# Kernel optimization log

Measured on AMD Instinct MI355X. Metric: run time of the kernel, lower is better.

The kernel has to match this reference:

```python
import jax, jax.numpy as jnp
import numpy as np
from math import sqrt


def setup_inputs() -> dict:
    key = jax.random.key(0)
    ks = jax.random.split(key, 5)
    B, S, D = 4, 2048, 1024
    scale = 0.02
    return {
        "x": jax.random.normal(ks[0], (B, S, D), dtype=jnp.float32),
        "Wq": jax.random.normal(ks[1], (D, D), dtype=jnp.float32) * scale,
        "Wk": jax.random.normal(ks[2], (D, D), dtype=jnp.float32) * scale,
        "Wv": jax.random.normal(ks[3], (D, D), dtype=jnp.float32) * scale,
        "Wo": jax.random.normal(ks[4], (D, D), dtype=jnp.float32) * scale,
    }


def reference(x, Wq, Wk, Wv, Wo):
    NUM_HEAD = 16
    B, S, D = x.shape
    d_k = D // NUM_HEAD

    # fused QKV projection: weights are (d_model, d_in), applied as W @ x^T -> x @ W^T
    q = jnp.einsum('od,bsd->bso', Wq, x)
    k = jnp.einsum('od,bsd->bso', Wk, x)
    v = jnp.einsum('od,bsd->bso', Wv, x)

    def split_heads(t):  # [B,S,D] -> [B,H,S,d_k]
        return t.reshape(B, S, NUM_HEAD, d_k).transpose(0, 2, 1, 3)

    q, k, v = split_heads(q), split_heads(k), split_heads(v)

    # naive causal attention: full [B,H,S,S] score matrix
    scores = jnp.einsum('bhqd,bhkd->bhqk', q, k) / sqrt(d_k)
    causal = jnp.tril(jnp.ones((S, S), dtype=bool))  # [S,S]
    scores = jnp.where(causal, scores, -jnp.inf)
    probs = jax.nn.softmax(scores, axis=-1)
    attn = jnp.einsum('bhqk,bhkd->bhqd', probs, v)

    # merge heads: [B,H,S,d_k] -> [B,S,D]
    attn = attn.transpose(0, 2, 1, 3).reshape(B, S, D)
    # output projection
    return jnp.einsum('om,bsm->bso', Wo, attn)
```

## Files before the change

### kernel.cpp

```cpp
#include <hip/hip_runtime.h>
#include <hip/hip_bf16.h>
#include <stdint.h>

typedef unsigned short u16;
typedef __attribute__((ext_vector_type(8))) short bf16x8;
typedef __attribute__((ext_vector_type(4))) float f32x4;
typedef __attribute__((ext_vector_type(16))) float f32x16;

#define AS1 __attribute__((address_space(1)))
#define AS3 __attribute__((address_space(3)))

__device__ __forceinline__ u16 f2bf(float f) {
  union { float f; uint32_t u; } v; v.f = f;
  uint32_t u = v.u;
  return (u16)((u + 0x7FFFu + ((u >> 16) & 1u)) >> 16);
}

__device__ __forceinline__ uint32_t cvtpk(float lo, float hi) {
  uint32_t d;
  asm("v_cvt_pk_bf16_f32 %0, %1, %2" : "=v"(d) : "v"(lo), "v"(hi));
  return d;
}

__global__ __launch_bounds__(256) void cvt_all_kernel(const float* __restrict__ x,
    const float* __restrict__ Wq, const float* __restrict__ Wk,
    const float* __restrict__ Wv, const float* __restrict__ Wo,
    u16* __restrict__ xb, u16* __restrict__ wqb, u16* __restrict__ wkb,
    u16* __restrict__ wvb, u16* __restrict__ wob) {
  const int bid = blockIdx.x;
  const float* s;
  u16* d;
  int i;
  if (bid < 8192) {
    s = x; d = xb; i = bid * 256 + threadIdx.x;
  } else {
    const int w = (bid - 8192) >> 10;
    i = ((bid - 8192) & 1023) * 256 + threadIdx.x;
    s = (w == 0) ? Wq : (w == 1) ? Wk : (w == 2) ? Wv : Wo;
    d = (w == 0) ? wqb : (w == 1) ? wkb : (w == 2) ? wvb : wob;
  }
  float4 v = reinterpret_cast<const float4*>(s)[i];
  uint2 o;
  o.x = cvtpk(v.x, v.y);
  o.y = cvtpk(v.z, v.w);
  reinterpret_cast<uint2*>(d)[i] = o;
}

#define QSCALE 0.18033688011112042f

#define GK 64

template <int MODE, int KC, typename OutT>
__device__ __forceinline__ void gemm128_body(u16* __restrict__ lds,
    const u16* __restrict__ A, const u16* __restrict__ Bm, OutT* __restrict__ C,
    int M, int N, int by, int bx, float oscale) {
  const int tid = threadIdx.x;
  const int lane = tid & 63;
  const int wave = tid >> 6;
  const int wm = wave >> 1, wn = wave & 1;
  const int l15 = lane & 15, lhi = lane >> 4;
  const int axor = (lane & 7) << 4;

  const int srow = tid >> 3;
  const int scol = (((tid & 7) ^ (srow & 7)) << 4);
  const size_t Kb = (size_t)KC * 2;
  const uint8_t* Ag = (const uint8_t*)A + (size_t)(by * 128 + srow) * Kb + scol;
  const uint8_t* Bg = (const uint8_t*)Bm + (size_t)(bx * 128 + srow) * Kb + scol;
  uint8_t* Lb = (uint8_t*)lds;

#define STG128(bufi, kt)                                                                  \
  do {                                                                                    \
    _Pragma("unroll") for (int c = 0; c < 4; ++c) {                                       \
      __builtin_amdgcn_global_load_lds(                                                   \
          (const AS1 uint32_t*)(Ag + (size_t)c * 32 * Kb + (size_t)(kt) * 128),           \
          (AS3 uint32_t*)(Lb + (bufi) * 32768 + c * 4096 + tid * 16), 16, 0, 0);          \
      __builtin_amdgcn_global_load_lds(                                                   \
          (const AS1 uint32_t*)(Bg + (size_t)c * 32 * Kb + (size_t)(kt) * 128),           \
          (AS3 uint32_t*)(Lb + (bufi) * 32768 + 16384 + c * 4096 + tid * 16), 16, 0, 0);  \
    }                                                                                     \
  } while (0)

  const f32x4 fzero = {0.f, 0.f, 0.f, 0.f};
  f32x4 acc[4][4];
#pragma unroll
  for (int m = 0; m < 4; ++m)
#pragma unroll
    for (int n = 0; n < 4; ++n) acc[m][n] = fzero;

  constexpr int NT = KC / GK;

  STG128(0, 0);
  STG128(1, 1);
  asm volatile("s_waitcnt vmcnt(8)" ::: "memory");
  __builtin_amdgcn_s_barrier();

#pragma unroll
  for (int t = 0; t < NT; ++t) {
    const int cur = t & 1;
    const uint8_t* Ab = Lb + cur * 32768;
    const uint8_t* Bb = Ab + 16384;
    bf16x8 aF[4][2], bF[4][2];
#pragma unroll
    for (int ff = 0; ff < 4; ++ff)
#pragma unroll
      for (int ks = 0; ks < 2; ++ks) {
        aF[ff][ks] = *reinterpret_cast<const bf16x8*>(
            Ab + (wm * 64 + ff * 16 + l15) * 128 + ((ks * 64 + lhi * 16) ^ axor));
        bF[ff][ks] = *reinterpret_cast<const bf16x8*>(
            Bb + (wn * 64 + ff * 16 + l15) * 128 + ((ks * 64 + lhi * 16) ^ axor));
      }
    if (t + 1 < NT) {
      asm volatile("s_waitcnt lgkmcnt(0)" ::: "memory");
      __builtin_amdgcn_sched_barrier(0);
      __builtin_amdgcn_s_barrier();
      if (t + 2 < NT) {
        STG128(cur, t + 2);
        asm volatile("s_waitcnt vmcnt(8)" ::: "memory");
      } else {
        asm volatile("s_waitcnt vmcnt(0)" ::: "memory");
      }
      __builtin_amdgcn_s_barrier();
    }
    __builtin_amdgcn_s_setprio(1);
#pragma unroll
    for (int mm = 0; mm < 4; ++mm)
#pragma unroll
      for (int nn = 0; nn < 4; ++nn)
#pragma unroll
        for (int ks = 0; ks < 2; ++ks)
          acc[mm][nn] = __builtin_amdgcn_mfma_f32_16x16x32_bf16(aF[mm][ks], bF[nn][ks],
                                                                acc[mm][nn], 0, 0, 0);
    __builtin_amdgcn_s_setprio(0);
  }

#pragma unroll
  for (int mf = 0; mf < 4; ++mf)
#pragma unroll
    for (int nf = 0; nf < 4; ++nf) {
      const int row0 = by * 128 + wm * 64 + mf * 16 + lhi * 4;
      const int col = bx * 128 + wn * 64 + nf * 16 + l15;
      if constexpr (MODE == 2) {
        uint2 pk;
        pk.x = cvtpk(acc[mf][nf][0], acc[mf][nf][1]);
        pk.y = cvtpk(acc[mf][nf][2], acc[mf][nf][3]);
        *reinterpret_cast<uint2*>((u16*)C + (size_t)col * M + row0) = pk;
      } else if constexpr (MODE == 1) {
#pragma unroll
        for (int r = 0; r < 4; ++r)
          ((float*)C)[(size_t)(row0 + r) * N + col] = acc[mf][nf][r];
      } else {
#pragma unroll
        for (int r = 0; r < 4; ++r)
          ((u16*)C)[(size_t)(row0 + r) * N + col] = f2bf(acc[mf][nf][r] * oscale);
      }
    }
#undef STG128
}

__global__ __launch_bounds__(256, 2) void gemm_qkv_kernel(const u16* __restrict__ A,
    const u16* __restrict__ W0, const u16* __restrict__ W1, const u16* __restrict__ W2,
    u16* __restrict__ OQ, u16* __restrict__ OK, u16* __restrict__ OVT, int M, int N) {
  __shared__ u16 lds[2][2][128 * GK];
  const int id = blockIdx.x;
  const int xcd = id & 7;
  const int slot = id >> 3;
  const int bz = slot >> 6;
  const int r = slot & 63;
  const int byi = r >> 3, bx = r & 7;
  const int by = xcd + 8 * byi;
  if (bz == 0)      gemm128_body<0, 1024, u16>(&lds[0][0][0], A, W0, OQ,  M, N, by, bx, QSCALE);
  else if (bz == 1) gemm128_body<0, 1024, u16>(&lds[0][0][0], A, W1, OK,  M, N, by, bx, 1.f);
  else              gemm128_body<2, 1024, u16>(&lds[0][0][0], A, W2, OVT, M, N, by, bx, 1.f);
}

__global__ __launch_bounds__(256, 2) void gemm_out_kernel(const u16* __restrict__ A,
    const u16* __restrict__ Bm, float* __restrict__ C, int M, int N) {
  __shared__ u16 lds[2][2][128 * GK];
  const int id = blockIdx.x;
  const int xcd = id & 7;
  const int slot = id >> 3;
  const int byi = slot >> 3, bx = slot & 7;
  const int by = xcd + 8 * byi;
  gemm128_body<1, 1024, float>(&lds[0][0][0], A, Bm, C, M, N, by, bx, 1.f);
}

#define KVB 64

template <int BUFB>
__device__ __forceinline__ void attn_bb(const uint8_t* const (&vb)[4],
    const bf16x8 (&qf)[4], f32x16 (&acc)[2], float& lrow,
    int kvb, int qr, bool boundary, int bb, int lh) {
  f32x16 sc;
#pragma unroll
  for (int r = 0; r < 16; ++r) sc[r] = 0.f;
  __builtin_amdgcn_s_setprio(1);
#pragma unroll
  for (int dc = 0; dc < 4; ++dc) {
    const bf16x8 kf = *reinterpret_cast<const bf16x8*>(vb[dc] + (BUFB * 16384 + bb * 4096));
    sc = __builtin_amdgcn_mfma_f32_32x32x16_bf16(kf, qf[dc], sc, 0, 0, 0);
  }
  __builtin_amdgcn_s_setprio(0);
  if (boundary) {
#pragma unroll
    for (int r = 0; r < 16; ++r) {
      const int kvg = kvb + (r & 3) + 8 * (r >> 2) + 4 * lh;
      sc[r] = (kvg > qr) ? -1e30f : sc[r];
    }
  }
#pragma unroll
  for (int r = 0; r < 16; ++r) sc[r] = __builtin_amdgcn_exp2f(sc[r]);
  float s0 = sc[0] + sc[8],  s1 = sc[1] + sc[9];
  float s2 = sc[2] + sc[10], s3 = sc[3] + sc[11];
  float s4 = sc[4] + sc[12], s5 = sc[5] + sc[13];
  float s6 = sc[6] + sc[14], s7 = sc[7] + sc[15];
  s0 += s4; s1 += s5; s2 += s6; s3 += s7;
  lrow += (s0 + s1) + (s2 + s3);
#pragma unroll
  for (int cc = 0; cc < 2; ++cc) {
    uint32_t a0 = cvtpk(sc[8 * cc + 0], sc[8 * cc + 1]);
    uint32_t a1 = cvtpk(sc[8 * cc + 2], sc[8 * cc + 3]);
    uint32_t b0 = cvtpk(sc[8 * cc + 4], sc[8 * cc + 5]);
    uint32_t b1 = cvtpk(sc[8 * cc + 6], sc[8 * cc + 7]);
    asm("v_permlane32_swap_b32 %0, %1" : "+v"(a0), "+v"(b0));
    asm("v_permlane32_swap_b32 %0, %1" : "+v"(a1), "+v"(b1));
    union { uint32_t u[4]; bf16x8 v8; } pf;
    pf.u[0] = a0; pf.u[1] = a1; pf.u[2] = b0; pf.u[3] = b1;
    const int c2 = bb * 2 + cc;
    __builtin_amdgcn_s_setprio(1);
#pragma unroll
    for (int db = 0; db < 2; ++db) {
      const bf16x8 vfg = *reinterpret_cast<const bf16x8*>(
          vb[c2] + (BUFB * 16384 + 8192 + db * 4096));
      acc[db] = __builtin_amdgcn_mfma_f32_32x32x16_bf16(vfg, pf.v8, acc[db], 0, 0, 0);
    }
    __builtin_amdgcn_s_setprio(0);
  }
}

__global__ __launch_bounds__(256, 4) void attn_kernel(const u16* __restrict__ Q,
    const u16* __restrict__ Kg, const u16* __restrict__ VTg, u16* __restrict__ O,
    int S, int H, int Dm, int T) {
  const int bh = blockIdx.x;
  const int b = bh / H, h = bh % H;
  const int s = 15 - blockIdx.y;
  const int q0 = 128 * s;
  const int tid = threadIdx.x;
  const int lane = tid & 63, wave = tid >> 6;
  const int l31 = lane & 31, lh = lane >> 5;

  __shared__ u16 KVs[2][2][64 * 64];

  const u16* Qh = Q + ((size_t)b * S) * Dm + h * 64;
  const u16* Kh = Kg + ((size_t)b * S) * Dm + h * 64;
  const u16* Vh = VTg + (size_t)(h * 64) * T + (size_t)b * S;
  const int qv = q0 + wave * 32;
  const int qr = qv + l31;

  bf16x8 qf[4];
#pragma unroll
  for (int dc = 0; dc < 4; ++dc)
    qf[dc] = *reinterpret_cast<const bf16x8*>(Qh + (size_t)qr * Dm + dc * 16 + lh * 8);

  const uint8_t* vb[4];
#pragma unroll
  for (int i = 0; i < 4; ++i)
    vb[i] = (const uint8_t*)KVs + l31 * 128 + ((((i * 2 + lh) ^ (l31 & 7))) << 4);

  f32x16 acc[2];
#pragma unroll
  for (int db = 0; db < 2; ++db)
#pragma unroll
    for (int r = 0; r < 16; ++r) acc[db][r] = 0.f;
  float lrow = 0.f;

#define STAGE(bufi, ti)                                                                        \
  do {                                                                                         \
    const int kvoff = (ti) * KVB;                                                              \
    const int sr = tid >> 3;                                                                   \
    const int sc_ = (((tid & 7) ^ (sr & 7)) << 3);                                             \
    _Pragma("unroll") for (int j = 0; j < 2; ++j) {                                            \
      __builtin_amdgcn_global_load_lds(                                                        \
          (const AS1 uint32_t*)(Kh + (size_t)(kvoff + j * 32 + sr) * Dm + sc_),                \
          (AS3 uint32_t*)(&KVs[bufi][0][j * 2048 + tid * 8]), 16, 0, 0);                       \
      __builtin_amdgcn_global_load_lds(                                                        \
          (const AS1 uint32_t*)(Vh + (size_t)(j * 32 + sr) * T + kvoff + sc_),                 \
          (AS3 uint32_t*)(&KVs[bufi][1][j * 2048 + tid * 8]), 16, 0, 0);                       \
    }                                                                                          \
  } while (0)

  const int nsi = s + 1;
  STAGE(0, 0);

  for (int si = 0; si < nsi; ++si) {
    const int t0 = 2 * si, t1 = 2 * si + 1;
    __syncthreads();
    STAGE(1, t1);
    {
      const int kv = t0 * KVB;
#pragma unroll
      for (int bb = 0; bb < 2; ++bb) {
        const int kvb = kv + bb * 32;
        if (kvb <= qv + 31)
          attn_bb<0>(vb, qf, acc, lrow, kvb, qr, (kvb + 31 > qv), bb, lh);
      }
    }
    __syncthreads();
    if (si + 1 < nsi) STAGE(0, t1 + 1);
    {
      const int kv = t1 * KVB;
#pragma unroll
      for (int bb = 0; bb < 2; ++bb) {
        const int kvb = kv + bb * 32;
        if (kvb <= qv + 31)
          attn_bb<1>(vb, qf, acc, lrow, kvb, qr, (kvb + 31 > qv), bb, lh);
      }
    }
  }

  lrow += __shfl_xor(lrow, 32, 64);
  const float inv = 1.f / lrow;
  __syncthreads();
  u16* Ost = &KVs[0][0][0];
  {
    const int row = wave * 32 + l31;
#pragma unroll
    for (int db = 0; db < 2; ++db)
#pragma unroll
      for (int g = 0; g < 4; ++g) {
        uint2 pk;
        pk.x = cvtpk(acc[db][4 * g + 0] * inv, acc[db][4 * g + 1] * inv);
        pk.y = cvtpk(acc[db][4 * g + 2] * inv, acc[db][4 * g + 3] * inv);
        const int blk = 4 * db + g;
        const int addr = row * 64 + (((blk ^ (row & 7)) << 3)) + 4 * lh;
        *reinterpret_cast<uint2*>(Ost + addr) = pk;
      }
  }
  __syncthreads();
#pragma unroll
  for (int p = 0; p < 4; ++p) {
    const int idx = p * 256 + tid;
    const int row = idx >> 3, seg = idx & 7;
    const float4 v = *reinterpret_cast<const float4*>(Ost + row * 64 + ((seg ^ (row & 7)) << 3));
    *reinterpret_cast<float4*>(O + ((size_t)b * S + q0 + row) * Dm + h * 64 + seg * 8) = v;
  }
#undef STAGE
}

extern "C" void kernel_launch(void* const* d_in, const int* in_sizes, int n_in,
                              void* d_out, int out_size, void* d_ws, size_t ws_size,
                              hipStream_t stream) {
  const float* x  = (const float*)d_in[0];
  const float* Wq = (const float*)d_in[1];
  const float* Wk = (const float*)d_in[2];
  const float* Wv = (const float*)d_in[3];
  const float* Wo = (const float*)d_in[4];
  float* out = (float*)d_out;

  const int B = 4, S = 2048, D = 1024, H = 16;
  const int T = B * S;

  uint8_t* p = (uint8_t*)d_ws;
  u16* xb  = (u16*)p; p += (size_t)T * D * 2;
  u16* wqb = (u16*)p; p += (size_t)D * D * 2;
  u16* wkb = (u16*)p; p += (size_t)D * D * 2;
  u16* wvb = (u16*)p; p += (size_t)D * D * 2;
  u16* wob = (u16*)p; p += (size_t)D * D * 2;
  u16* Qb  = (u16*)p; p += (size_t)T * D * 2;
  u16* Kb  = (u16*)p; p += (size_t)T * D * 2;
  u16* VTb = (u16*)p; p += (size_t)D * T * 2;
  u16* Ab  = xb;

  cvt_all_kernel<<<dim3(12288), dim3(256), 0, stream>>>(x, Wq, Wk, Wv, Wo,
                                                        xb, wqb, wkb, wvb, wob);

  gemm_qkv_kernel<<<dim3(1536), dim3(256), 0, stream>>>(xb, wqb, wkb, wvb, Qb, Kb, VTb, T, D);

  attn_kernel<<<dim3(B * H, 16), dim3(256), 0, stream>>>(Qb, Kb, VTb, Ab, S, H, D, T);

  gemm_out_kernel<<<dim3(512), dim3(256), 0, stream>>>(Ab, wob, out, T, D);
}
```

Baseline: 126.5 us.

## Use 256x256 tiles with 8 waves and interleaved pipeline for QKV GEMM

Replaces the 128x128 QKV projection GEMM with a 256x256 tile kernel of 512 threads, 8 waves each computing 128x64, and 128KB of double-buffered LDS. Global-to-LDS loads are split into half-tiles and interleaved with four MFMA quadrants per k-step, with barriers and setprio around them. The larger tile is meant to raise arithmetic intensity and cut redundant global and LDS traffic. In exchange it uses one block per CU, launches only 384 blocks, and adds many barriers, which lowers occupancy and leaves a partial last wave.

Measured after the change: 138.7 us. 9.6% more time.

```diff
diff --git a/kernel.cpp b/kernel.cpp
--- a/kernel.cpp
+++ b/kernel.cpp
@@ -48,6 +48,167 @@
 
 #define QSCALE 0.18033688011112042f
 
+template <int MODE, int KC, typename OutT>
+__device__ __forceinline__ void gemm256_body(u16* __restrict__ lds_,
+    const u16* __restrict__ A, const u16* __restrict__ Bm, OutT* __restrict__ C,
+    int M, int N, int by, int bx, float oscale) {
+  const int tid = threadIdx.x;
+  const int lane = tid & 63;
+  const int wave = tid >> 6;
+  const int wm = wave >> 2, wn = wave & 3;
+  const int l15 = lane & 15, lhi = lane >> 4;
+  const int axor = (l15 & 7) << 4;
+
+  const int srow = tid >> 3;
+  const int scol = (((tid & 7) ^ (srow & 7)) << 4);
+  const size_t Kb = (size_t)KC * 2;
+  const uint8_t* Ag = (const uint8_t*)A + (size_t)(by * 256 + srow) * Kb + scol;
+  const uint8_t* Bg = (const uint8_t*)Bm + (size_t)(bx * 256 + srow) * Kb + scol;
+  uint8_t* Lb = (uint8_t*)lds_;
+
+#define STGH(bufi, kt, reg, h)                                                            \
+  do {                                                                                    \
+    const uint8_t* gb = (reg) ? Bg : Ag;                                                  \
+    _Pragma("unroll") for (int c = 0; c < 2; ++c) {                                       \
+      __builtin_amdgcn_global_load_lds(                                                   \
+          (const AS1 uint32_t*)(gb + (size_t)((h) * 128 + c * 64) * Kb +                  \
+                                (size_t)(kt) * 128),                                      \
+          (AS3 uint32_t*)(Lb + (bufi) * 65536 + (reg) * 32768 + (h) * 16384 +             \
+                          c * 8192 + tid * 16), 16, 0, 0);                                \
+    }                                                                                     \
+  } while (0)
+
+#define RD_A(bufi, mh)                                                                    \
+  do {                                                                                    \
+    _Pragma("unroll") for (int mm = 0; mm < 4; ++mm)                                      \
+      _Pragma("unroll") for (int ks = 0; ks < 2; ++ks)                                    \
+        aF[mm][ks] = *reinterpret_cast<const bf16x8*>(                                    \
+            Lb + (bufi) * 65536 + (wm * 128 + (mh) * 64 + mm * 16 + l15) * 128 +          \
+            ((ks * 64 + lhi * 16) ^ axor));                                               \
+  } while (0)
+
+#define RD_B(bufi, nh)                                                                    \
+  do {                                                                                    \
+    _Pragma("unroll") for (int nn = 0; nn < 2; ++nn)                                      \
+      _Pragma("unroll") for (int ks = 0; ks < 2; ++ks)                                    \
+        bF[nn][ks] = *reinterpret_cast<const bf16x8*>(                                    \
+            Lb + (bufi) * 65536 + 32768 + (wn * 64 + (nh) * 32 + nn * 16 + l15) * 128 +   \
+            ((ks * 64 + lhi * 16) ^ axor));                                               \
+  } while (0)
+
+#define MFMA_Q(mh, nh)                                                                    \
+  do {                                                                                    \
+    asm volatile("s_waitcnt lgkmcnt(0)" ::: "memory");                                    \
+    __builtin_amdgcn_sched_barrier(0);                                                    \
+    __builtin_amdgcn_s_setprio(1);                                                        \
+    _Pragma("unroll") for (int mm = 0; mm < 4; ++mm)                                      \
+      _Pragma("unroll") for (int nn = 0; nn < 2; ++nn)                                    \
+        _Pragma("unroll") for (int ks = 0; ks < 2; ++ks)                                  \
+          acc[(mh) * 4 + mm][(nh) * 2 + nn] = __builtin_amdgcn_mfma_f32_16x16x32_bf16(    \
+              aF[mm][ks], bF[nn][ks], acc[(mh) * 4 + mm][(nh) * 2 + nn], 0, 0, 0);        \
+    __builtin_amdgcn_s_setprio(0);                                                        \
+  } while (0)
+
+#define BAR() __builtin_amdgcn_s_barrier()
+
+  const f32x4 fzero = {0.f, 0.f, 0.f, 0.f};
+  f32x4 acc[8][4];
+#pragma unroll
+  for (int m = 0; m < 8; ++m)
+#pragma unroll
+    for (int n = 0; n < 4; ++n) acc[m][n] = fzero;
+
+  constexpr int NT = KC / 64;
+  constexpr int NITER = NT / 2;
+
+  STGH(0, 0, 0, 0); STGH(0, 0, 0, 1); STGH(0, 0, 1, 0); STGH(0, 0, 1, 1);
+  STGH(1, 1, 0, 0);
+  asm volatile("s_waitcnt vmcnt(2)" ::: "memory");
+  BAR();
+
+  bf16x8 aF[4][2], bF[2][2];
+  for (int i = 0; i < NITER; ++i) {
+    const int ta = 2 * i, tb = 2 * i + 1;
+    const bool g = (i + 1 < NITER);
+
+    RD_A(0, 0); RD_B(0, 0);
+    STGH(1, tb, 0, 1);
+    BAR(); MFMA_Q(0, 0); BAR();
+    RD_B(0, 1);
+    STGH(1, tb, 1, 0);
+    BAR(); MFMA_Q(0, 1); BAR();
+    RD_A(0, 1);
+    STGH(1, tb, 1, 1);
+    BAR(); MFMA_Q(1, 1); BAR();
+    RD_B(0, 0);
+    if (g) STGH(0, ta + 2, 0, 0);
+    BAR(); MFMA_Q(1, 0);
+    if (g) asm volatile("s_waitcnt vmcnt(2)" ::: "memory");
+    else   asm volatile("s_waitcnt vmcnt(0)" ::: "memory");
+    BAR();
+
+    RD_A(1, 0); RD_B(1, 0);
+    if (g) STGH(0, ta + 2, 0, 1);
+    BAR(); MFMA_Q(0, 0); BAR();
+    RD_B(1, 1);
+    if (g) STGH(0, ta + 2, 1, 0);
+    BAR(); MFMA_Q(0, 1); BAR();
+    RD_A(1, 1);
+    if (g) STGH(0, ta + 2, 1, 1);
+    BAR(); MFMA_Q(1, 1); BAR();
+    RD_B(1, 0);
+    if (g) STGH(1, tb + 2, 0, 0);
+    BAR(); MFMA_Q(1, 0);
+    if (g) asm volatile("s_waitcnt vmcnt(2)" ::: "memory");
+    else   asm volatile("s_waitcnt vmcnt(0)" ::: "memory");
+    BAR();
+  }
+
+#pragma unroll
+  for (int mf = 0; mf < 8; ++mf)
+#pragma unroll
+    for (int nf = 0; nf < 4; ++nf) {
+      const int row0 = by * 256 + wm * 128 + mf * 16 + lhi * 4;
+      const int col = bx * 256 + wn * 64 + nf * 16 + l15;
+      if constexpr (MODE == 2) {
+        uint2 pk;
+        pk.x = cvtpk(acc[mf][nf][0], acc[mf][nf][1]);
+        pk.y = cvtpk(acc[mf][nf][2], acc[mf][nf][3]);
+        *reinterpret_cast<uint2*>((u16*)C + (size_t)col * M + row0) = pk;
+      } else if constexpr (MODE == 1) {
+#pragma unroll
+        for (int r = 0; r < 4; ++r)
+          ((float*)C)[(size_t)(row0 + r) * N + col] = acc[mf][nf][r];
+      } else {
+#pragma unroll
+        for (int r = 0; r < 4; ++r)
+          ((u16*)C)[(size_t)(row0 + r) * N + col] = f2bf(acc[mf][nf][r] * oscale);
+      }
+    }
+#undef STGH
+#undef RD_A
+#undef RD_B
+#undef MFMA_Q
+#undef BAR
+}
+
+__global__ __launch_bounds__(512) void gemm_qkv_kernel(const u16* __restrict__ A,
+    const u16* __restrict__ W0, const u16* __restrict__ W1, const u16* __restrict__ W2,
+    u16* __restrict__ OQ, u16* __restrict__ OK, u16* __restrict__ OVT, int M, int N) {
+  __shared__ u16 lds[2][2][256 * 64];
+  const int id = blockIdx.x;
+  const int xcd = id & 7;
+  const int slot = id >> 3;
+  const int byi = slot / 12;
+  const int c = slot - byi * 12;
+  const int bx = c & 3;
+  const int bz = c >> 2;
+  const int by = xcd + 8 * byi;
+  if (bz == 0)      gemm256_body<0, 1024, u16>(&lds[0][0][0], A, W0, OQ,  M, N, by, bx, QSCALE);
+  else if (bz == 1) gemm256_body<0, 1024, u16>(&lds[0][0][0], A, W1, OK,  M, N, by, bx, 1.f);
+  else              gemm256_body<2, 1024, u16>(&lds[0][0][0], A, W2, OVT, M, N, by, bx, 1.f);
+}
+
 #define GK 64
 
 template <int MODE, int KC, typename OutT>
@@ -155,22 +316,6 @@
       }
     }
 #undef STG128
-}
-
-__global__ __launch_bounds__(256, 2) void gemm_qkv_kernel(const u16* __restrict__ A,
-    const u16* __restrict__ W0, const u16* __restrict__ W1, const u16* __restrict__ W2,
-    u16* __restrict__ OQ, u16* __restrict__ OK, u16* __restrict__ OVT, int M, int N) {
-  __shared__ u16 lds[2][2][128 * GK];
-  const int id = blockIdx.x;
-  const int xcd = id & 7;
-  const int slot = id >> 3;
-  const int bz = slot >> 6;
-  const int r = slot & 63;
-  const int byi = r >> 3, bx = r & 7;
-  const int by = xcd + 8 * byi;
-  if (bz == 0)      gemm128_body<0, 1024, u16>(&lds[0][0][0], A, W0, OQ,  M, N, by, bx, QSCALE);
-  else if (bz == 1) gemm128_body<0, 1024, u16>(&lds[0][0][0], A, W1, OK,  M, N, by, bx, 1.f);
-  else              gemm128_body<2, 1024, u16>(&lds[0][0][0], A, W2, OVT, M, N, by, bx, 1.f);
 }
 
 __global__ __launch_bounds__(256, 2) void gemm_out_kernel(const u16* __restrict__ A,
@@ -373,7 +518,7 @@
   cvt_all_kernel<<<dim3(12288), dim3(256), 0, stream>>>(x, Wq, Wk, Wv, Wo,
                                                         xb, wqb, wkb, wvb, wob);
 
-  gemm_qkv_kernel<<<dim3(1536), dim3(256), 0, stream>>>(xb, wqb, wkb, wvb, Qb, Kb, VTb, T, D);
+  gemm_qkv_kernel<<<dim3(384), dim3(512), 0, stream>>>(xb, wqb, wkb, wvb, Qb, Kb, VTb, T, D);
 
   attn_kernel<<<dim3(B * H, 16), dim3(256), 0, stream>>>(Qb, Kb, VTb, Ab, S, H, D, T);
 
```

## Fuse Q/K/V projections into one GEMM tile sharing the A operand

Applied to the files above, without the earlier changes.

Replaces the three separate 128x128 QKV GEMM tiles with one kernel where each block loads a 128-row x tile once and multiplies it against 64-column slices of Wq, Wk and Wv together. This cuts the repeated global and LDS traffic for the activation operand and drops the grid from 1536 to 1024 blocks. In exchange the kernel needs 80KB of LDS and 24 accumulator fragments per wave, which may lower occupancy below the requested 2 blocks per CU. The old MODE 2 path in the shared GEMM body is removed.

After: 127.5 us. No clear change (+0.7%).

```diff
diff --git a/kernel.cpp b/kernel.cpp
--- a/kernel.cpp
+++ b/kernel.cpp
@@ -48,6 +48,122 @@
 
 #define QSCALE 0.18033688011112042f
 
+__global__ __launch_bounds__(256, 2) void gemm_qkv_kernel(const u16* __restrict__ A,
+    const u16* __restrict__ W0, const u16* __restrict__ W1, const u16* __restrict__ W2,
+    u16* __restrict__ OQ, u16* __restrict__ OK, u16* __restrict__ OVT, int M, int N) {
+  __shared__ __align__(16) uint8_t SMEM[81920];
+  const int id = blockIdx.x;
+  const int xcd = id & 7;
+  const int slot = id >> 3;
+  const int byi = slot >> 4;
+  const int bx = slot & 15;
+  const int by = xcd + 8 * byi;
+
+  const int tid = threadIdx.x;
+  const int lane = tid & 63;
+  const int wave = tid >> 6;
+  const int wm = wave >> 1, wn = wave & 1;
+  const int l15 = lane & 15, lhi = lane >> 4;
+  const int axor = (lane & 7) << 4;
+
+  const int srow = tid >> 3;
+  const int scol = (((tid & 7) ^ (srow & 7)) << 4);
+  const size_t Kb = 1024 * 2;
+  const uint8_t* Ag  = (const uint8_t*)A  + (size_t)(by * 128 + srow) * Kb + scol;
+  const uint8_t* Bg0 = (const uint8_t*)W0 + (size_t)(bx * 64 + srow) * Kb + scol;
+  const uint8_t* Bg1 = (const uint8_t*)W1 + (size_t)(bx * 64 + srow) * Kb + scol;
+  const uint8_t* Bg2 = (const uint8_t*)W2 + (size_t)(bx * 64 + srow) * Kb + scol;
+  uint8_t* Lb = SMEM;
+
+#define STGF(bufi, kt)                                                                    \
+  do {                                                                                    \
+    _Pragma("unroll") for (int c = 0; c < 4; ++c)                                         \
+      __builtin_amdgcn_global_load_lds(                                                   \
+          (const AS1 uint32_t*)(Ag + (size_t)c * 32 * Kb + (size_t)(kt) * 128),           \
+          (AS3 uint32_t*)(Lb + (bufi) * 40960 + c * 4096 + tid * 16), 16, 0, 0);          \
+    _Pragma("unroll") for (int c = 0; c < 2; ++c) {                                       \
+      __builtin_amdgcn_global_load_lds(                                                   \
+          (const AS1 uint32_t*)(Bg0 + (size_t)c * 32 * Kb + (size_t)(kt) * 128),          \
+          (AS3 uint32_t*)(Lb + (bufi) * 40960 + 16384 + c * 4096 + tid * 16), 16, 0, 0);  \
+      __builtin_amdgcn_global_load_lds(                                                   \
+          (const AS1 uint32_t*)(Bg1 + (size_t)c * 32 * Kb + (size_t)(kt) * 128),          \
+          (AS3 uint32_t*)(Lb + (bufi) * 40960 + 24576 + c * 4096 + tid * 16), 16, 0, 0);  \
+      __builtin_amdgcn_global_load_lds(                                                   \
+          (const AS1 uint32_t*)(Bg2 + (size_t)c * 32 * Kb + (size_t)(kt) * 128),          \
+          (AS3 uint32_t*)(Lb + (bufi) * 40960 + 32768 + c * 4096 + tid * 16), 16, 0, 0);  \
+    }                                                                                     \
+  } while (0)
+
+  const f32x4 fzero = {0.f, 0.f, 0.f, 0.f};
+  f32x4 acc[3][4][2];
+#pragma unroll
+  for (int w = 0; w < 3; ++w)
+#pragma unroll
+    for (int m = 0; m < 4; ++m)
+#pragma unroll
+      for (int n = 0; n < 2; ++n) acc[w][m][n] = fzero;
+
+  constexpr int NT = 16;
+
+  STGF(0, 0);
+  __syncthreads();
+
+#pragma unroll
+  for (int t = 0; t < NT; ++t) {
+    const int cur = t & 1;
+    if (t + 1 < NT) STGF(cur ^ 1, t + 1);
+    const uint8_t* Ab = Lb + cur * 40960;
+    bf16x8 aF[4][2];
+#pragma unroll
+    for (int mf = 0; mf < 4; ++mf)
+#pragma unroll
+      for (int ks = 0; ks < 2; ++ks)
+        aF[mf][ks] = *reinterpret_cast<const bf16x8*>(
+            Ab + (wm * 64 + mf * 16 + l15) * 128 + ((ks * 64 + lhi * 16) ^ axor));
+#pragma unroll
+    for (int w = 0; w < 3; ++w) {
+      const uint8_t* Bb = Ab + 16384 + w * 8192;
+      bf16x8 bF[2][2];
+#pragma unroll
+      for (int nf = 0; nf < 2; ++nf)
+#pragma unroll
+        for (int ks = 0; ks < 2; ++ks)
+          bF[nf][ks] = *reinterpret_cast<const bf16x8*>(
+              Bb + (wn * 32 + nf * 16 + l15) * 128 + ((ks * 64 + lhi * 16) ^ axor));
+      __builtin_amdgcn_s_setprio(1);
+#pragma unroll
+      for (int mm = 0; mm < 4; ++mm)
+#pragma unroll
+        for (int nn = 0; nn < 2; ++nn)
+#pragma unroll
+          for (int ks = 0; ks < 2; ++ks)
+            acc[w][mm][nn] = __builtin_amdgcn_mfma_f32_16x16x32_bf16(
+                aF[mm][ks], bF[nn][ks], acc[w][mm][nn], 0, 0, 0);
+      __builtin_amdgcn_s_setprio(0);
+    }
+    __syncthreads();
+  }
+
+#pragma unroll
+  for (int mf = 0; mf < 4; ++mf)
+#pragma unroll
+    for (int nf = 0; nf < 2; ++nf) {
+      const int row0 = by * 128 + wm * 64 + mf * 16 + lhi * 4;
+      const int col = bx * 64 + wn * 32 + nf * 16 + l15;
+#pragma unroll
+      for (int r = 0; r < 4; ++r)
+        OQ[(size_t)(row0 + r) * N + col] = f2bf(acc[0][mf][nf][r] * QSCALE);
+#pragma unroll
+      for (int r = 0; r < 4; ++r)
+        OK[(size_t)(row0 + r) * N + col] = f2bf(acc[1][mf][nf][r]);
+      uint2 pk;
+      pk.x = cvtpk(acc[2][mf][nf][0], acc[2][mf][nf][1]);
+      pk.y = cvtpk(acc[2][mf][nf][2], acc[2][mf][nf][3]);
+      *reinterpret_cast<uint2*>(OVT + (size_t)col * M + row0) = pk;
+    }
+#undef STGF
+}
+
 #define GK 64
 
 template <int MODE, int KC, typename OutT>
@@ -139,12 +255,7 @@
     for (int nf = 0; nf < 4; ++nf) {
       const int row0 = by * 128 + wm * 64 + mf * 16 + lhi * 4;
       const int col = bx * 128 + wn * 64 + nf * 16 + l15;
-      if constexpr (MODE == 2) {
-        uint2 pk;
-        pk.x = cvtpk(acc[mf][nf][0], acc[mf][nf][1]);
-        pk.y = cvtpk(acc[mf][nf][2], acc[mf][nf][3]);
-        *reinterpret_cast<uint2*>((u16*)C + (size_t)col * M + row0) = pk;
-      } else if constexpr (MODE == 1) {
+      if constexpr (MODE == 1) {
 #pragma unroll
         for (int r = 0; r < 4; ++r)
           ((float*)C)[(size_t)(row0 + r) * N + col] = acc[mf][nf][r];
@@ -155,22 +266,6 @@
       }
     }
 #undef STG128
-}
-
-__global__ __launch_bounds__(256, 2) void gemm_qkv_kernel(const u16* __restrict__ A,
-    const u16* __restrict__ W0, const u16* __restrict__ W1, const u16* __restrict__ W2,
-    u16* __restrict__ OQ, u16* __restrict__ OK, u16* __restrict__ OVT, int M, int N) {
-  __shared__ u16 lds[2][2][128 * GK];
-  const int id = blockIdx.x;
-  const int xcd = id & 7;
-  const int slot = id >> 3;
-  const int bz = slot >> 6;
-  const int r = slot & 63;
-  const int byi = r >> 3, bx = r & 7;
-  const int by = xcd + 8 * byi;
-  if (bz == 0)      gemm128_body<0, 1024, u16>(&lds[0][0][0], A, W0, OQ,  M, N, by, bx, QSCALE);
-  else if (bz == 1) gemm128_body<0, 1024, u16>(&lds[0][0][0], A, W1, OK,  M, N, by, bx, 1.f);
-  else              gemm128_body<2, 1024, u16>(&lds[0][0][0], A, W2, OVT, M, N, by, bx, 1.f);
 }
 
 __global__ __launch_bounds__(256, 2) void gemm_out_kernel(const u16* __restrict__ A,
@@ -373,7 +468,7 @@
   cvt_all_kernel<<<dim3(12288), dim3(256), 0, stream>>>(x, Wq, Wk, Wv, Wo,
                                                         xb, wqb, wkb, wvb, wob);
 
-  gemm_qkv_kernel<<<dim3(1536), dim3(256), 0, stream>>>(xb, wqb, wkb, wvb, Qb, Kb, VTb, T, D);
+  gemm_qkv_kernel<<<dim3(1024), dim3(256), 0, stream>>>(xb, wqb, wkb, wvb, Qb, Kb, VTb, T, D);
 
   attn_kernel<<<dim3(B * H, 16), dim3(256), 0, stream>>>(Qb, Kb, VTb, Ab, S, H, D, T);
 
```
